# Optimization experiments

Hardware: AMD Instinct MI355X
Metric: run time of the kernel (lower is better)

## Reference

```python
import jax, jax.numpy as jnp
import numpy as np

NUM_CLASSES = 1000
Z_DIM = 256
BATCH = 16384


def setup_inputs() -> dict:
    key = jax.random.key(0)
    k1, k2, k3 = jax.random.split(key, 3)
    x = jax.random.normal(k1, (BATCH, Z_DIM), dtype=jnp.float32)
    centers = jax.random.normal(k2, (NUM_CLASSES, Z_DIM), dtype=jnp.float32)
    labels = jax.random.randint(k3, (BATCH,), 0, NUM_CLASSES, dtype=jnp.int64)
    return {"x": x, "centers": centers, "labels": labels}


def reference(x, centers, labels):
    B, C = x.shape[0], centers.shape[0]
    distmat = (
        jnp.sum(x * x, axis=1, keepdims=True)
        + jnp.sum(centers * centers, axis=1)[None, :]
        - 2.0 * jnp.einsum("bd,cd->bc", x, centers)
    )
    # original gathers distances to NON-matching classes (kk = 1 - mask),
    # exactly C-1 entries per row, then sqrt, clamp, and global mean.
    mask = labels[:, None] == jnp.arange(C, dtype=labels.dtype)[None, :]  # True where class == label
    d = jnp.clip(jnp.sqrt(distmat), 1e-8, 1e8)
    total = jnp.sum(jnp.where(mask, 0.0, d))
    loss = total / (B * (C - 1))
    return loss
```

## Files before the change

### kernel.cpp

```cpp
#include <hip/hip_runtime.h>

#define BATCH 16384
#define ZDIM  256
#define NCLS  1000
#define NPAD  1024

typedef __bf16 bf16x8 __attribute__((ext_vector_type(8)));
typedef float  f32x4  __attribute__((ext_vector_type(4)));

#define WS_XB   0
#define WS_CB   8388608
#define WS_XSQ  8912896
#define WS_CSQ  8978432
#define WS_PART 8982528

__device__ __forceinline__ unsigned short f2bf(float f) {
    union { float f; unsigned int u; } v; v.f = f;
    unsigned int u = v.u;
    unsigned int r = (u + 0x7fffu + ((u >> 16) & 1u)) >> 16;
    return (unsigned short)r;
}

__global__ void prep(const float* __restrict__ x,
                     const float* __restrict__ centers,
                     unsigned short* __restrict__ xb,
                     unsigned short* __restrict__ cb,
                     float* __restrict__ xsq,
                     float* __restrict__ csq) {
    const int wid  = threadIdx.x >> 6;
    const int lane = threadIdx.x & 63;
    const int lr   = lane & 15;
    const int quad = lane >> 4;

    if (blockIdx.x < 256) {
        const int mt = blockIdx.x * 4 + wid;
        const float* src = x + (size_t)(mt * 16 + lr) * ZDIM + quad * 8;
        float s = 0.0f;
        #pragma unroll
        for (int kt = 0; kt < 8; ++kt) {
            const float4 a = *(const float4*)(src + kt * 32);
            const float4 b = *(const float4*)(src + kt * 32 + 4);
            s += a.x*a.x + a.y*a.y + a.z*a.z + a.w*a.w
               + b.x*b.x + b.y*b.y + b.z*b.z + b.w*b.w;
            unsigned short* dst = xb + ((size_t)(mt * 8 + kt) * 64 + lane) * 8;
            ushort4 lo, hi;
            lo.x = f2bf(a.x); lo.y = f2bf(a.y); lo.z = f2bf(a.z); lo.w = f2bf(a.w);
            hi.x = f2bf(b.x); hi.y = f2bf(b.y); hi.z = f2bf(b.z); hi.w = f2bf(b.w);
            *(ushort4*)dst       = lo;
            *(ushort4*)(dst + 4) = hi;
        }
        s += __shfl_xor(s, 16);
        s += __shfl_xor(s, 32);
        if (lane < 16) xsq[mt * 16 + lane] = s;
    } else {
        const int ct  = (blockIdx.x - 256) * 4 + wid;
        const int row = ct * 16 + lr;
        const bool ok = (row < NCLS);
        const float* src = centers + (size_t)row * ZDIM + quad * 8;
        float s = 0.0f;
        #pragma unroll
        for (int kt = 0; kt < 8; ++kt) {
            float4 a = {0,0,0,0}, b = {0,0,0,0};
            if (ok) {
                a = *(const float4*)(src + kt * 32);
                b = *(const float4*)(src + kt * 32 + 4);
            }
            s += a.x*a.x + a.y*a.y + a.z*a.z + a.w*a.w
               + b.x*b.x + b.y*b.y + b.z*b.z + b.w*b.w;
            unsigned short* dst = cb + ((size_t)(ct * 8 + kt) * 64 + lane) * 8;
            ushort4 lo, hi;
            lo.x = f2bf(a.x); lo.y = f2bf(a.y); lo.z = f2bf(a.z); lo.w = f2bf(a.w);
            hi.x = f2bf(b.x); hi.y = f2bf(b.y); hi.z = f2bf(b.z); hi.w = f2bf(b.w);
            *(ushort4*)dst       = lo;
            *(ushort4*)(dst + 4) = hi;
        }
        s += __shfl_xor(s, 16);
        s += __shfl_xor(s, 32);
        if (lane < 16) csq[ct * 16 + lane] = s;
    }
}

__global__ __launch_bounds__(256, 3) void gemm_loss(
        const unsigned short* __restrict__ xb,
        const unsigned short* __restrict__ cb,
        const float* __restrict__ xsq,
        const float* __restrict__ csq,
        const int* __restrict__ labels,
        float* __restrict__ part) {
    __shared__ float xsq_s[128];
    __shared__ float csq_s[128];
    __shared__ int   lab_s[128];
    __shared__ float wsum[4];

    const int tid  = threadIdx.x;
    const int lane = tid & 63;
    const int wid  = tid >> 6;
    const int bm   = blockIdx.x & 127;
    const int bn   = blockIdx.x >> 7;
    const int m0   = bm * 128;
    const int n0   = bn * 128;

    if (tid < 128) {
        xsq_s[tid] = xsq[m0 + tid];
        lab_s[tid] = labels[m0 + tid];
    } else {
        const int t = tid - 128;
        csq_s[t] = csq[n0 + t];
    }

    const int wm = wid & 1;
    const int wn = wid >> 1;

    f32x4 acc_r[4][4];
    #pragma unroll
    for (int i = 0; i < 4; ++i)
        #pragma unroll
        for (int j = 0; j < 4; ++j) {
            f32x4 z = {0.0f, 0.0f, 0.0f, 0.0f};
            acc_r[i][j] = z;
        }

    const int mtb = bm * 8 + wm * 4;
    const int ctb = bn * 8 + wn * 4;
    const bf16x8* __restrict__ A = (const bf16x8*)xb;
    const bf16x8* __restrict__ B = (const bf16x8*)cb;

    #pragma unroll
    for (int kt = 0; kt < 8; ++kt) {
        bf16x8 af[4], bfr[4];
        #pragma unroll
        for (int i = 0; i < 4; ++i)
            af[i] = A[(size_t)((mtb + i) * 8 + kt) * 64 + lane];
        #pragma unroll
        for (int j = 0; j < 4; ++j)
            bfr[j] = B[(size_t)((ctb + j) * 8 + kt) * 64 + lane];
        #pragma unroll
        for (int i = 0; i < 4; ++i)
            #pragma unroll
            for (int j = 0; j < 4; ++j)
                acc_r[i][j] = __builtin_amdgcn_mfma_f32_16x16x32_bf16(
                    af[i], bfr[j], acc_r[i][j], 0, 0, 0);
    }

    __syncthreads();

    const int quad = lane >> 4;
    const int lr   = lane & 15;
    float sum = 0.0f;
    #pragma unroll
    for (int j = 0; j < 4; ++j) {
        const int col_l = wn * 64 + j * 16 + lr;
        const int col_g = n0 + col_l;
        const float cs = csq_s[col_l];
        const bool colok = (col_g < NCLS);
        #pragma unroll
        for (int i = 0; i < 4; ++i) {
            #pragma unroll
            for (int r = 0; r < 4; ++r) {
                const int row_l = wm * 64 + i * 16 + quad * 4 + r;
                float dist = xsq_s[row_l] + cs - 2.0f * acc_r[i][j][r];
                float d = sqrtf(fmaxf(dist, 0.0f));
                d = fminf(fmaxf(d, 1e-8f), 1e8f);
                if (colok && (lab_s[row_l] != col_g)) sum += d;
            }
        }
    }

    #pragma unroll
    for (int off = 32; off; off >>= 1) sum += __shfl_down(sum, off);
    if (lane == 0) wsum[wid] = sum;
    __syncthreads();
    if (tid == 0) part[blockIdx.x] = wsum[0] + wsum[1] + wsum[2] + wsum[3];
}

__global__ void finalize(const float* __restrict__ part, float* __restrict__ out) {
    const int tid  = threadIdx.x;
    const int lane = tid & 63;
    const int wid  = tid >> 6;
    __shared__ float wsum[4];
    float s = part[tid] + part[tid + 256] + part[tid + 512] + part[tid + 768];
    #pragma unroll
    for (int off = 32; off; off >>= 1) s += __shfl_down(s, off);
    if (lane == 0) wsum[wid] = s;
    __syncthreads();
    if (tid == 0)
        out[0] = (wsum[0] + wsum[1] + wsum[2] + wsum[3]) * (1.0f / (16384.0f * 999.0f));
}

extern "C" void kernel_launch(void* const* d_in, const int* in_sizes, int n_in,
                              void* d_out, int out_size, void* d_ws, size_t ws_size,
                              hipStream_t stream) {
    const float* x       = (const float*)d_in[0];
    const float* centers = (const float*)d_in[1];
    const int*   labels  = (const int*)d_in[2];
    float*       out     = (float*)d_out;

    char* ws = (char*)d_ws;
    unsigned short* xb   = (unsigned short*)(ws + WS_XB);
    unsigned short* cb   = (unsigned short*)(ws + WS_CB);
    float*          xsq  = (float*)(ws + WS_XSQ);
    float*          csq  = (float*)(ws + WS_CSQ);
    float*          part = (float*)(ws + WS_PART);

    prep<<<272, 256, 0, stream>>>(x, centers, xb, cb, xsq, csq);
    gemm_loss<<<(BATCH / 128) * (NPAD / 128), 256, 0, stream>>>(
        xb, cb, xsq, csq, labels, part);
    finalize<<<1, 256, 0, stream>>>(part, out);
}
```

Baseline: 92.24 us.

## Switch GEMM to FP8 MFMA with LDS-staged 256x256 tiles

Quantizes x and centers to FP8 (e4m3) in the prep kernel instead of bf16 and uses the fp8 16x16x32 MFMA. The GEMM now uses 512-thread blocks on 256x256 tiles, staging operands through LDS via global_load_lds in two K halves, with 256 blocks in total. The finalize kernel is adjusted for 256 partial sums. This halves the intermediate traffic and raises per-block reuse, but FP8 quantization of the dot products introduces much larger error in the distances, which may exceed the tolerance.

```diff
diff --git a/kernel.cpp b/kernel.cpp
--- a/kernel.cpp
+++ b/kernel.cpp
@@ -5,26 +5,28 @@
 #define NCLS  1000
 #define NPAD  1024
 
-typedef __bf16 bf16x8 __attribute__((ext_vector_type(8)));
-typedef float  f32x4  __attribute__((ext_vector_type(4)));
-
-#define WS_XB   0
-#define WS_CB   8388608
-#define WS_XSQ  8912896
-#define WS_CSQ  8978432
-#define WS_PART 8982528
-
-__device__ __forceinline__ unsigned short f2bf(float f) {
-    union { float f; unsigned int u; } v; v.f = f;
-    unsigned int u = v.u;
-    unsigned int r = (u + 0x7fffu + ((u >> 16) & 1u)) >> 16;
-    return (unsigned short)r;
+typedef float f32x4 __attribute__((ext_vector_type(4)));
+
+#define WS_XQ   0
+#define WS_CQ   4194304
+#define WS_XSQ  4456448
+#define WS_CSQ  4521984
+#define WS_PART 4526080
+
+#define GLOAD_LDS(gp, lp)                                                     \
+    __builtin_amdgcn_global_load_lds(                                         \
+        (__attribute__((address_space(1))) const void*)(gp),                  \
+        (__attribute__((address_space(3))) void*)(lp), 16, 0, 0)
+
+template <bool W>
+__device__ __forceinline__ int pk2fp8(float a, float b, int old) {
+    return __builtin_amdgcn_cvt_pk_fp8_f32(a, b, old, W);
 }
 
 __global__ void prep(const float* __restrict__ x,
                      const float* __restrict__ centers,
-                     unsigned short* __restrict__ xb,
-                     unsigned short* __restrict__ cb,
+                     char* __restrict__ xq,
+                     char* __restrict__ cq,
                      float* __restrict__ xsq,
                      float* __restrict__ csq) {
     const int wid  = threadIdx.x >> 6;
@@ -42,12 +44,10 @@
             const float4 b = *(const float4*)(src + kt * 32 + 4);
             s += a.x*a.x + a.y*a.y + a.z*a.z + a.w*a.w
                + b.x*b.x + b.y*b.y + b.z*b.z + b.w*b.w;
-            unsigned short* dst = xb + ((size_t)(mt * 8 + kt) * 64 + lane) * 8;
-            ushort4 lo, hi;
-            lo.x = f2bf(a.x); lo.y = f2bf(a.y); lo.z = f2bf(a.z); lo.w = f2bf(a.w);
-            hi.x = f2bf(b.x); hi.y = f2bf(b.y); hi.z = f2bf(b.z); hi.w = f2bf(b.w);
-            *(ushort4*)dst       = lo;
-            *(ushort4*)(dst + 4) = hi;
+            int lo = pk2fp8<false>(a.x, a.y, 0); lo = pk2fp8<true>(a.z, a.w, lo);
+            int hi = pk2fp8<false>(b.x, b.y, 0); hi = pk2fp8<true>(b.z, b.w, hi);
+            int2 v; v.x = lo; v.y = hi;
+            *(int2*)(xq + ((size_t)(mt * 8 + kt) * 64 + lane) * 8) = v;
         }
         s += __shfl_xor(s, 16);
         s += __shfl_xor(s, 32);
@@ -67,12 +67,10 @@
             }
             s += a.x*a.x + a.y*a.y + a.z*a.z + a.w*a.w
                + b.x*b.x + b.y*b.y + b.z*b.z + b.w*b.w;
-            unsigned short* dst = cb + ((size_t)(ct * 8 + kt) * 64 + lane) * 8;
-            ushort4 lo, hi;
-            lo.x = f2bf(a.x); lo.y = f2bf(a.y); lo.z = f2bf(a.z); lo.w = f2bf(a.w);
-            hi.x = f2bf(b.x); hi.y = f2bf(b.y); hi.z = f2bf(b.z); hi.w = f2bf(b.w);
-            *(ushort4*)dst       = lo;
-            *(ushort4*)(dst + 4) = hi;
+            int lo = pk2fp8<false>(a.x, a.y, 0); lo = pk2fp8<true>(a.z, a.w, lo);
+            int hi = pk2fp8<false>(b.x, b.y, 0); hi = pk2fp8<true>(b.z, b.w, hi);
+            int2 v; v.x = lo; v.y = hi;
+            *(int2*)(cq + ((size_t)(ct * 8 + kt) * 64 + lane) * 8) = v;
         }
         s += __shfl_xor(s, 16);
         s += __shfl_xor(s, 32);
@@ -80,85 +78,104 @@
     }
 }
 
-__global__ __launch_bounds__(256, 3) void gemm_loss(
-        const unsigned short* __restrict__ xb,
-        const unsigned short* __restrict__ cb,
+__global__ __launch_bounds__(512, 2) void gemm_loss(
+        const char* __restrict__ xq,
+        const char* __restrict__ cq,
         const float* __restrict__ xsq,
         const float* __restrict__ csq,
         const int* __restrict__ labels,
         float* __restrict__ part) {
-    __shared__ float xsq_s[128];
-    __shared__ float csq_s[128];
-    __shared__ int   lab_s[128];
-    __shared__ float wsum[4];
+    __shared__ char smem[65536];
 
     const int tid  = threadIdx.x;
     const int lane = tid & 63;
     const int wid  = tid >> 6;
-    const int bm   = blockIdx.x & 127;
-    const int bn   = blockIdx.x >> 7;
-    const int m0   = bm * 128;
-    const int n0   = bn * 128;
-
-    if (tid < 128) {
+    const int bm   = blockIdx.x & 63;
+    const int bn   = blockIdx.x >> 6;
+    const int m0   = bm * 256;
+    const int n0   = bn * 256;
+    const int wr   = wid & 3;
+    const int wc   = wid >> 2;
+
+    f32x4 acc_r[4][8];
+    #pragma unroll
+    for (int i = 0; i < 4; ++i)
+        #pragma unroll
+        for (int j = 0; j < 8; ++j) {
+            f32x4 z = {0.0f, 0.0f, 0.0f, 0.0f};
+            acc_r[i][j] = z;
+        }
+
+    const long long* AL = (const long long*)smem;
+    const long long* BL = (const long long*)(smem + 32768);
+
+    #pragma unroll
+    for (int h = 0; h < 2; ++h) {
+        #pragma unroll
+        for (int it = 0; it < 4; ++it) {
+            const int c = it * 512 + tid;
+            const int mtile = c >> 7, kt4 = (c >> 5) & 3, pair = c & 31;
+            const char* g = xq + (size_t)((bm * 16 + mtile) * 8 + h * 4 + kt4) * 512
+                               + pair * 16;
+            GLOAD_LDS(g, smem + c * 16);
+        }
+        #pragma unroll
+        for (int it = 0; it < 4; ++it) {
+            const int c = it * 512 + tid;
+            const int ctile = c >> 7, kt4 = (c >> 5) & 3, pair = c & 31;
+            const char* g = cq + (size_t)((bn * 16 + ctile) * 8 + h * 4 + kt4) * 512
+                               + pair * 16;
+            GLOAD_LDS(g, smem + 32768 + c * 16);
+        }
+        __syncthreads();
+
+        #pragma unroll
+        for (int kt4 = 0; kt4 < 4; ++kt4) {
+            long long af[4], bf[8];
+            #pragma unroll
+            for (int mi = 0; mi < 4; ++mi)
+                af[mi] = AL[((wr * 4 + mi) * 4 + kt4) * 64 + lane];
+            #pragma unroll
+            for (int nj = 0; nj < 8; ++nj)
+                bf[nj] = BL[((wc * 8 + nj) * 4 + kt4) * 64 + lane];
+            #pragma unroll
+            for (int mi = 0; mi < 4; ++mi)
+                #pragma unroll
+                for (int nj = 0; nj < 8; ++nj)
+                    acc_r[mi][nj] = __builtin_amdgcn_mfma_f32_16x16x32_fp8_fp8(
+                        af[mi], bf[nj], acc_r[mi][nj], 0, 0, 0);
+        }
+        __syncthreads();
+    }
+
+    float* xsq_s = (float*)smem;
+    float* csq_s = (float*)(smem + 1024);
+    int*   lab_s = (int*)(smem + 2048);
+    float* wsum  = (float*)(smem + 3072);
+    if (tid < 256) {
         xsq_s[tid] = xsq[m0 + tid];
         lab_s[tid] = labels[m0 + tid];
     } else {
-        const int t = tid - 128;
+        const int t = tid - 256;
         csq_s[t] = csq[n0 + t];
     }
-
-    const int wm = wid & 1;
-    const int wn = wid >> 1;
-
-    f32x4 acc_r[4][4];
-    #pragma unroll
-    for (int i = 0; i < 4; ++i)
-        #pragma unroll
-        for (int j = 0; j < 4; ++j) {
-            f32x4 z = {0.0f, 0.0f, 0.0f, 0.0f};
-            acc_r[i][j] = z;
-        }
-
-    const int mtb = bm * 8 + wm * 4;
-    const int ctb = bn * 8 + wn * 4;
-    const bf16x8* __restrict__ A = (const bf16x8*)xb;
-    const bf16x8* __restrict__ B = (const bf16x8*)cb;
-
-    #pragma unroll
-    for (int kt = 0; kt < 8; ++kt) {
-        bf16x8 af[4], bfr[4];
-        #pragma unroll
-        for (int i = 0; i < 4; ++i)
-            af[i] = A[(size_t)((mtb + i) * 8 + kt) * 64 + lane];
-        #pragma unroll
-        for (int j = 0; j < 4; ++j)
-            bfr[j] = B[(size_t)((ctb + j) * 8 + kt) * 64 + lane];
-        #pragma unroll
-        for (int i = 0; i < 4; ++i)
-            #pragma unroll
-            for (int j = 0; j < 4; ++j)
-                acc_r[i][j] = __builtin_amdgcn_mfma_f32_16x16x32_bf16(
-                    af[i], bfr[j], acc_r[i][j], 0, 0, 0);
-    }
-
     __syncthreads();
 
     const int quad = lane >> 4;
     const int lr   = lane & 15;
     float sum = 0.0f;
     #pragma unroll
-    for (int j = 0; j < 4; ++j) {
-        const int col_l = wn * 64 + j * 16 + lr;
+    for (int nj = 0; nj < 8; ++nj) {
+        const int col_l = wc * 128 + nj * 16 + lr;
         const int col_g = n0 + col_l;
         const float cs = csq_s[col_l];
         const bool colok = (col_g < NCLS);
         #pragma unroll
-        for (int i = 0; i < 4; ++i) {
+        for (int mi = 0; mi < 4; ++mi) {
             #pragma unroll
             for (int r = 0; r < 4; ++r) {
-                const int row_l = wm * 64 + i * 16 + quad * 4 + r;
-                float dist = xsq_s[row_l] + cs - 2.0f * acc_r[i][j][r];
+                const int row_l = wr * 64 + mi * 16 + quad * 4 + r;
+                float dist = xsq_s[row_l] + cs - 2.0f * acc_r[mi][nj][r];
                 float d = sqrtf(fmaxf(dist, 0.0f));
                 d = fminf(fmaxf(d, 1e-8f), 1e8f);
                 if (colok && (lab_s[row_l] != col_g)) sum += d;
@@ -170,7 +187,12 @@
     for (int off = 32; off; off >>= 1) sum += __shfl_down(sum, off);
     if (lane == 0) wsum[wid] = sum;
     __syncthreads();
-    if (tid == 0) part[blockIdx.x] = wsum[0] + wsum[1] + wsum[2] + wsum[3];
+    if (tid == 0) {
+        float t = 0.0f;
+        #pragma unroll
+        for (int w = 0; w < 8; ++w) t += wsum[w];
+        part[blockIdx.x] = t;
+    }
 }
 
 __global__ void finalize(const float* __restrict__ part, float* __restrict__ out) {
@@ -178,7 +200,7 @@
     const int lane = tid & 63;
     const int wid  = tid >> 6;
     __shared__ float wsum[4];
-    float s = part[tid] + part[tid + 256] + part[tid + 512] + part[tid + 768];
+    float s = part[tid];
     #pragma unroll
     for (int off = 32; off; off >>= 1) s += __shfl_down(s, off);
     if (lane == 0) wsum[wid] = s;
@@ -196,14 +218,13 @@
     float*       out     = (float*)d_out;
 
     char* ws = (char*)d_ws;
-    unsigned short* xb   = (unsigned short*)(ws + WS_XB);
-    unsigned short* cb   = (unsigned short*)(ws + WS_CB);
-    float*          xsq  = (float*)(ws + WS_XSQ);
-    float*          csq  = (float*)(ws + WS_CSQ);
-    float*          part = (float*)(ws + WS_PART);
-
-    prep<<<272, 256, 0, stream>>>(x, centers, xb, cb, xsq, csq);
-    gemm_loss<<<(BATCH / 128) * (NPAD / 128), 256, 0, stream>>>(
-        xb, cb, xsq, csq, labels, part);
+    char*  xq   = ws + WS_XQ;
+    char*  cq   = ws + WS_CQ;
+    float* xsq  = (float*)(ws + WS_XSQ);
+    float* csq  = (float*)(ws + WS_CSQ);
+    float* part = (float*)(ws + WS_PART);
+
+    prep<<<272, 256, 0, stream>>>(x, centers, xq, cq, xsq, csq);
+    gemm_loss<<<256, 512, 0, stream>>>(xq, cq, xsq, csq, labels, part);
     finalize<<<1, 256, 0, stream>>>(part, out);
 }
```

New measurement: 94.57 us. 2.5% more time.
